# Kernel tuning notes

Measured on AMD Instinct MI355X. Metric: run time of the kernel, lower is better.

## Reference

```python
import jax, jax.numpy as jnp
import numpy as np

D = 1024
ITERATIONS = 2


def setup_inputs() -> dict:
    key = jax.random.key(0)
    ks = jax.random.split(key, 7)
    s = 1.0 / np.sqrt(D)  # PyTorch GRUCell/Linear init scale
    x = jax.random.normal(ks[0], (8, 4096, D), dtype=jnp.float32)
    W_ih = jax.random.uniform(ks[1], (3 * D, D), minval=-s, maxval=s, dtype=jnp.float32)
    W_hh = jax.random.uniform(ks[2], (3 * D, D), minval=-s, maxval=s, dtype=jnp.float32)
    b_ih = jax.random.uniform(ks[3], (3 * D,), minval=-s, maxval=s, dtype=jnp.float32)
    b_hh = jax.random.uniform(ks[4], (3 * D,), minval=-s, maxval=s, dtype=jnp.float32)
    We = jax.random.uniform(ks[5], (1, D), minval=-s, maxval=s, dtype=jnp.float32)
    be = jax.random.uniform(ks[6], (1,), minval=-s, maxval=s, dtype=jnp.float32)
    return {"x": x, "W_ih": W_ih, "W_hh": W_hh, "b_ih": b_ih, "b_hh": b_hh, "We": We, "be": be}


def _gru_cell(inp, h, W_ih, W_hh, b_ih, b_hh):
    # PyTorch GRUCell gate order: r, z, n
    gi = inp @ W_ih.T + b_ih  # [N, 3D]
    gh = h @ W_hh.T + b_hh    # [N, 3D]
    i_r, i_z, i_n = jnp.split(gi, 3, axis=-1)
    h_r, h_z, h_n = jnp.split(gh, 3, axis=-1)
    r = jax.nn.sigmoid(i_r + h_r)
    z = jax.nn.sigmoid(i_z + h_z)
    n = jnp.tanh(i_n + r * h_n)
    return (1.0 - z) * n + z * h


def reference(x, W_ih, W_hh, b_ih, b_hh, We, be):
    B, S, Dm = x.shape
    state = x.reshape(-1, Dm)  # [B*S, D]
    for _ in range(ITERATIONS):
        error = jax.nn.sigmoid(state @ We.T + be)  # [B*S, 1]
        new_state = _gru_cell(state, state, W_ih, W_hh, b_ih, b_hh)
        state = (1.0 - error) * state + error * new_state
    return state.reshape(B, S, Dm)
```

## Files before the change

kernel.cpp:

```cpp
#include <hip/hip_runtime.h>

#define DD 1024

typedef int   i32x4  __attribute__((ext_vector_type(4)));
typedef int   i32x8  __attribute__((ext_vector_type(8)));
typedef float f32x16 __attribute__((ext_vector_type(16)));

__device__ __forceinline__ float sigm(float x) { return 1.0f / (1.0f + __expf(-x)); }
__device__ __forceinline__ float tanh_fast(float x) {
  float e = __expf(-2.0f * fabsf(x));
  float t = (1.0f - e) / (1.0f + e);
  return copysignf(t, x);
}
__device__ __forceinline__ void gload_lds16(const void* g, void* l) {
  __builtin_amdgcn_global_load_lds((const __attribute__((address_space(1))) void*)g,
                                   (__attribute__((address_space(3))) void*)l, 16, 0, 0);
}
__device__ __forceinline__ unsigned pk_fp8x4(float a, float b, float c, float d) {
  int u = __builtin_amdgcn_cvt_pk_fp8_f32(a, b, 0, false);
  u = __builtin_amdgcn_cvt_pk_fp8_f32(c, d, u, true);
  return (unsigned)u;
}


__global__ __launch_bounds__(256) void prep_weights(
    const float* __restrict__ Wih, const float* __restrict__ Whh,
    const float* __restrict__ bih, const float* __restrict__ bhh,
    unsigned char* __restrict__ Wcat8, float* __restrict__ bias) {
  int i = blockIdx.x * 256 + threadIdx.x;
  int g = i >> 18;
  int rem = i & 262143;
  int n = rem >> 8;
  int k4 = rem & 255;
  const float4* wih4 = reinterpret_cast<const float4*>(Wih);
  const float4* whh4 = reinterpret_cast<const float4*>(Whh);
  float4 v;
  if (g == 0) {
    size_t idx = (size_t)n * 256 + k4;
    float4 a = wih4[idx], b = whh4[idx];
    v = make_float4(a.x + b.x, a.y + b.y, a.z + b.z, a.w + b.w);
  } else if (g == 1) {
    size_t idx = (size_t)(DD + n) * 256 + k4;
    float4 a = wih4[idx], b = whh4[idx];
    v = make_float4(a.x + b.x, a.y + b.y, a.z + b.z, a.w + b.w);
  } else if (g == 2) {
    size_t idx = (size_t)(2 * DD + n) * 256 + k4;
    v = wih4[idx];
  } else {
    size_t idx = (size_t)(2 * DD + n) * 256 + k4;
    v = whh4[idx];
  }
  unsigned pkd = pk_fp8x4(v.x * 32.0f, v.y * 32.0f, v.z * 32.0f, v.w * 32.0f);

  int db  = n >> 5;
  int n_t = g * 32 + (n & 31);
  size_t addr = (size_t)db * 131072 + (size_t)(k4 >> 4) * 8192 +
                (n_t >> 3) * 512 + ((k4 >> 2) & 3) * 128 + (n_t & 7) * 16 +
                (k4 & 3) * 4;
  *reinterpret_cast<unsigned*>(Wcat8 + addr) = pkd;

  if (i < 4 * DD) {
    int bg = i >> 10, bn = i & 1023;
    float bv;
    if (bg == 0)      bv = bih[bn] + bhh[bn];
    else if (bg == 1) bv = bih[DD + bn] + bhh[DD + bn];
    else if (bg == 2) bv = bih[2 * DD + bn];
    else              bv = bhh[2 * DD + bn];
    bias[i] = bv;
  }
}

__global__ __launch_bounds__(256) void error_cast(
    const float* S, const float* __restrict__ We, const float* __restrict__ be,
    unsigned char* __restrict__ Sb8, float* __restrict__ err) {
  __shared__ float part[4];
  const int row = blockIdx.x;
  const int t = threadIdx.x;
  float4 v = reinterpret_cast<const float4*>(S + (size_t)row * DD)[t];
  float4 w = reinterpret_cast<const float4*>(We)[t];
  float dot = v.x * w.x + v.y * w.y + v.z * w.z + v.w * w.w;

  int r = row & 127;
  size_t addr = (size_t)(row >> 7) * 131072 + (size_t)(t >> 4) * 8192 +
                (r >> 3) * 512 + ((t >> 2) & 3) * 128 + (r & 7) * 16 +
                (t & 3) * 4;
  *reinterpret_cast<unsigned*>(Sb8 + addr) = pk_fp8x4(v.x, v.y, v.z, v.w);

#pragma unroll
  for (int off = 32; off > 0; off >>= 1) dot += __shfl_xor(dot, off);
  if ((t & 63) == 0) part[t >> 6] = dot;
  __syncthreads();
  if (t == 0) err[row] = sigm(part[0] + part[1] + part[2] + part[3] + be[0]);
}

__global__ __launch_bounds__(256, 4) void gru_fused_gemm(
    const unsigned char* __restrict__ Sb8,
    const unsigned char* __restrict__ Wcat8,
    const float* __restrict__ bias,
    const float* __restrict__ err,
    const float* Sf,
    float* out, int M) {
  __shared__ alignas(16) unsigned char As[2 * 8192];
  __shared__ alignas(16) unsigned char Bs[2 * 8192];

  const int bid = blockIdx.x;
  const int x = bid & 7;
  const int c = bid >> 3;
  const int db = (x & 1) * 16 + (c & 15);
  const int rb = (x >> 1) * 64 + (c >> 4);

  const int tid = threadIdx.x;
  const int w = tid >> 6;
  const int lane = tid & 63;
  const int l31 = lane & 31;
  const int h = lane >> 5;

  const unsigned char* sA0 = Sb8 + (size_t)rb * 131072 + (size_t)w * 1024 + lane * 16;
  const unsigned char* sB0 = Wcat8 + (size_t)db * 131072 + (size_t)w * 1024 + lane * 16;
  unsigned char* const dA0 = As + w * 1024;
  unsigned char* const dB0 = Bs + w * 1024;

  const int ar = w * 32 + l31;
  const int aoff = (ar >> 3) * 512 + (2 * h) * 128 + (ar & 7) * 16;
  int boff[4];
#pragma unroll
  for (int g = 0; g < 4; ++g) {
    int br = g * 32 + l31;
    boff[g] = (br >> 3) * 512 + (2 * h) * 128 + (br & 7) * 16;
  }

  f32x16 acc[4];
#pragma unroll
  for (int g = 0; g < 4; ++g)
#pragma unroll
    for (int r = 0; r < 16; ++r) acc[g][r] = 0.0f;

  auto stage = [&](int t) {
    const int slot = (t & 1) * 8192;
    const size_t koff = (size_t)t * 8192;
    gload_lds16(sA0 + koff, dA0 + slot);
    gload_lds16(sA0 + koff + 4096, dA0 + slot + 4096);
    gload_lds16(sB0 + koff, dB0 + slot);
    gload_lds16(sB0 + koff + 4096, dB0 + slot + 4096);
  };

  stage(0);
  stage(1);

#pragma unroll
  for (int t = 0; t < 16; ++t) {
    const int sb = (t & 1) * 8192;
    if (t < 15) asm volatile("s_waitcnt vmcnt(4)" ::: "memory");
    else        asm volatile("s_waitcnt vmcnt(0)" ::: "memory");
    __builtin_amdgcn_s_barrier();

    const unsigned char* Ab = As + sb;
    const unsigned char* Bb = Bs + sb;
    i32x4 a0 = *reinterpret_cast<const i32x4*>(Ab + aoff);
    i32x4 a1 = *reinterpret_cast<const i32x4*>(Ab + aoff + 128);
    i32x8 a = __builtin_shufflevector(a0, a1, 0, 1, 2, 3, 4, 5, 6, 7);
    i32x8 bf[4];
#pragma unroll
    for (int g = 0; g < 4; ++g) {
      i32x4 b0 = *reinterpret_cast<const i32x4*>(Bb + boff[g]);
      i32x4 b1 = *reinterpret_cast<const i32x4*>(Bb + boff[g] + 128);
      bf[g] = __builtin_shufflevector(b0, b1, 0, 1, 2, 3, 4, 5, 6, 7);
    }
    asm volatile("s_waitcnt lgkmcnt(0)" ::: "memory");
    __builtin_amdgcn_s_barrier();

    if (t <= 13) stage(t + 2);

    __builtin_amdgcn_s_setprio(1);
#pragma unroll
    for (int g = 0; g < 4; ++g)
      acc[g] = __builtin_amdgcn_mfma_scale_f32_32x32x64_f8f6f4(
          a, bf[g], acc[g], 0, 0, 0, 127, 0, 122);
    __builtin_amdgcn_s_setprio(0);
  }

  const int dgcol = db * 32 + l31;
  const float b_r = bias[dgcol];
  const float b_z = bias[DD + dgcol];
  const float b_i = bias[2 * DD + dgcol];
  const float b_h = bias[3 * DD + dgcol];
#pragma unroll
  for (int reg = 0; reg < 16; ++reg) {
    int rowf = (reg & 3) + 8 * (reg >> 2) + 4 * h;
    int m = rb * 128 + w * 32 + rowf;
    float e = err[m];
    float hh = Sf[(size_t)m * DD + dgcol];
    float r = sigm(acc[0][reg] + b_r);
    float z = sigm(acc[1][reg] + b_z);
    float n = tanh_fast(acc[2][reg] + b_i + r * (acc[3][reg] + b_h));
    out[(size_t)m * DD + dgcol] = hh + e * (1.0f - z) * (n - hh);
  }
}

extern "C" void kernel_launch(void* const* d_in, const int* in_sizes, int n_in,
                              void* d_out, int out_size, void* d_ws, size_t ws_size,
                              hipStream_t stream) {
  const float* x   = (const float*)d_in[0];
  const float* Wih = (const float*)d_in[1];
  const float* Whh = (const float*)d_in[2];
  const float* bih = (const float*)d_in[3];
  const float* bhh = (const float*)d_in[4];
  const float* We  = (const float*)d_in[5];
  const float* be  = (const float*)d_in[6];
  float* out = (float*)d_out;
  const int M = in_sizes[0] / DD;

  char* ws = (char*)d_ws;
  unsigned char* Sb8   = (unsigned char*)ws;
  unsigned char* Wcat8 = (unsigned char*)(ws + (size_t)M * DD);
  float* bias = (float*)(ws + (size_t)M * DD + (size_t)4 * DD * DD);
  float* err  = (float*)(ws + (size_t)M * DD + (size_t)4 * DD * DD + (size_t)4 * DD * 4);

  prep_weights<<<4096, 256, 0, stream>>>(Wih, Whh, bih, bhh, Wcat8, bias);

  const int nwg = (M / 128) * 32;
  const float* S = x;
  for (int it = 0; it < 2; ++it) {
    error_cast<<<M, 256, 0, stream>>>(S, We, be, Sb8, err);
    gru_fused_gemm<<<nwg, 256, 0, stream>>>(Sb8, Wcat8, bias, err, S, out, M);
    S = out;
  }
}
```

Measured before the change: 438.6 us.

## Fuse next-iteration fp8 cast and error dot product into first GEMM epilogue

The first GRU GEMM epilogue now writes the fp8 tiled copy of the new state and per-column-block partial dot products with We, so the second iteration no longer needs the error_cast pass that rereads the full fp32 state. A small sigmoid_err kernel reduces the 32 partials per row. This removes a full-state read and one launch, but adds byte-granular scattered fp8 stores and shuffle reductions in the epilogue, and needs a second fp8 buffer in the workspace, with a fallback path when the workspace is too small.

```diff
diff --git a/kernel.cpp b/kernel.cpp
--- a/kernel.cpp
+++ b/kernel.cpp
@@ -93,13 +93,30 @@
   if (t == 0) err[row] = sigm(part[0] + part[1] + part[2] + part[3] + be[0]);
 }
 
+__global__ __launch_bounds__(256) void sigmoid_err(
+    const float* __restrict__ errp, const float* __restrict__ be,
+    float* __restrict__ err, int M) {
+  int m = blockIdx.x * 256 + threadIdx.x;
+  if (m >= M) return;
+  const float4* p = reinterpret_cast<const float4*>(errp + (size_t)m * 32);
+  float s = 0.f;
+#pragma unroll
+  for (int i = 0; i < 8; ++i) { float4 q = p[i]; s += q.x + q.y + q.z + q.w; }
+  err[m] = sigm(s + be[0]);
+}
+
+template <bool FUSE>
 __global__ __launch_bounds__(256, 4) void gru_fused_gemm(
     const unsigned char* __restrict__ Sb8,
     const unsigned char* __restrict__ Wcat8,
     const float* __restrict__ bias,
     const float* __restrict__ err,
     const float* Sf,
-    float* out, int M) {
+    float* out,
+    const float* __restrict__ We,
+    float* __restrict__ errp,
+    unsigned char* __restrict__ SbOut,
+    int M) {
   __shared__ alignas(16) unsigned char As[2 * 8192];
   __shared__ alignas(16) unsigned char Bs[2 * 8192];
 
@@ -184,6 +201,12 @@
   const float b_z = bias[DD + dgcol];
   const float b_i = bias[2 * DD + dgcol];
   const float b_h = bias[3 * DD + dgcol];
+  float We_c = 0.f;
+  size_t kpart = 0;
+  if constexpr (FUSE) {
+    We_c = We[dgcol];
+    kpart = (size_t)(dgcol >> 6) * 8192 + ((dgcol >> 4) & 3) * 128 + (dgcol & 15);
+  }
 #pragma unroll
   for (int reg = 0; reg < 16; ++reg) {
     int rowf = (reg & 3) + 8 * (reg >> 2) + 4 * h;
@@ -193,7 +216,20 @@
     float r = sigm(acc[0][reg] + b_r);
     float z = sigm(acc[1][reg] + b_z);
     float n = tanh_fast(acc[2][reg] + b_i + r * (acc[3][reg] + b_h));
-    out[(size_t)m * DD + dgcol] = hh + e * (1.0f - z) * (n - hh);
+    float o = hh + e * (1.0f - z) * (n - hh);
+    out[(size_t)m * DD + dgcol] = o;
+    if constexpr (FUSE) {
+      int rr = m & 127;
+      SbOut[(size_t)(m >> 7) * 131072 + kpart + (rr >> 3) * 512 + (rr & 7) * 16] =
+          (unsigned char)(__builtin_amdgcn_cvt_pk_fp8_f32(o, o, 0, false) & 0xFF);
+      float v = o * We_c;
+      v += __shfl_xor(v, 1);
+      v += __shfl_xor(v, 2);
+      v += __shfl_xor(v, 4);
+      v += __shfl_xor(v, 8);
+      v += __shfl_xor(v, 16);
+      if (l31 == 0) errp[(size_t)m * 32 + db] = v;
+    }
   }
 }
 
@@ -209,20 +245,45 @@
   const float* be  = (const float*)d_in[6];
   float* out = (float*)d_out;
   const int M = in_sizes[0] / DD;
+  const int nwg = (M / 128) * 32;
 
   char* ws = (char*)d_ws;
-  unsigned char* Sb8   = (unsigned char*)ws;
-  unsigned char* Wcat8 = (unsigned char*)(ws + (size_t)M * DD);
-  float* bias = (float*)(ws + (size_t)M * DD + (size_t)4 * DD * DD);
-  float* err  = (float*)(ws + (size_t)M * DD + (size_t)4 * DD * DD + (size_t)4 * DD * 4);
-
-  prep_weights<<<4096, 256, 0, stream>>>(Wih, Whh, bih, bhh, Wcat8, bias);
-
-  const int nwg = (M / 128) * 32;
-  const float* S = x;
-  for (int it = 0; it < 2; ++it) {
-    error_cast<<<M, 256, 0, stream>>>(S, We, be, Sb8, err);
-    gru_fused_gemm<<<nwg, 256, 0, stream>>>(Sb8, Wcat8, bias, err, S, out, M);
-    S = out;
-  }
-}
+  const size_t SZ_IMG = (size_t)M * DD;
+  const size_t off_SbB  = SZ_IMG;
+  const size_t off_W    = 2 * SZ_IMG;
+  const size_t off_bias = off_W + 4194304;
+  const size_t off_errp = off_bias + 16384;
+  const size_t off_err  = off_errp + (size_t)M * 32 * 4;
+  const size_t need_full = off_err + (size_t)M * 4;
+
+  if (ws_size >= need_full) {
+    unsigned char* SbA   = (unsigned char*)ws;
+    unsigned char* SbB   = (unsigned char*)(ws + off_SbB);
+    unsigned char* Wcat8 = (unsigned char*)(ws + off_W);
+    float* bias = (float*)(ws + off_bias);
+    float* errp = (float*)(ws + off_errp);
+    float* err  = (float*)(ws + off_err);
+
+    prep_weights<<<4096, 256, 0, stream>>>(Wih, Whh, bih, bhh, Wcat8, bias);
+    error_cast<<<M, 256, 0, stream>>>(x, We, be, SbA, err);
+    gru_fused_gemm<true><<<nwg, 256, 0, stream>>>(SbA, Wcat8, bias, err, x, out,
+                                                  We, errp, SbB, M);
+    sigmoid_err<<<(M + 255) / 256, 256, 0, stream>>>(errp, be, err, M);
+    gru_fused_gemm<false><<<nwg, 256, 0, stream>>>(SbB, Wcat8, bias, err, out, out,
+                                                   nullptr, nullptr, nullptr, M);
+  } else {
+    unsigned char* SbA   = (unsigned char*)ws;
+    unsigned char* Wcat8 = (unsigned char*)(ws + SZ_IMG);
+    float* bias = (float*)(ws + SZ_IMG + 4194304);
+    float* err  = (float*)(ws + SZ_IMG + 4194304 + 16384);
+
+    prep_weights<<<4096, 256, 0, stream>>>(Wih, Whh, bih, bhh, Wcat8, bias);
+    const float* S = x;
+    for (int it = 0; it < 2; ++it) {
+      error_cast<<<M, 256, 0, stream>>>(S, We, be, SbA, err);
+      gru_fused_gemm<false><<<nwg, 256, 0, stream>>>(SbA, Wcat8, bias, err, S, out,
+                                                     nullptr, nullptr, nullptr, M);
+      S = out;
+    }
+  }
+}
```

New measurement: 478.3 us. 1.09x slower.
